# Kernel tuning notes

Measured on AMD Instinct MI355X. Metric: run time of the kernel, lower is better.

The kernel has to match this reference:

```python
import jax, jax.numpy as jnp
import numpy as np

B, T, C = 8, 2048, 1024
EPS = 1e-6
NEG_INF = -2.0**32 + 1.0


def setup_inputs() -> dict:
    key = jax.random.key(0)
    ks = jax.random.split(key, 10)
    glorot = lambda k, shape: jax.random.normal(k, shape, jnp.float32) * np.sqrt(2.0 / (shape[0] + shape[1]))
    return {
        "queries": jax.random.normal(ks[0], (B, T, C), jnp.float32),
        "keys": jax.random.normal(ks[1], (B, T, C), jnp.float32),
        "key_masks": jnp.ones((B, T), jnp.float32),
        "query_masks": jnp.ones((B, T), jnp.float32),
        "u": glorot(ks[2], (C, C)),
        # d = GlorotNormal([C,C]) * eye(C) -> only the diagonal matters
        "d_diag": jnp.diag(glorot(ks[3], (C, C))),
        "W1": glorot(ks[4], (C, C)),
        "b1": jnp.zeros((C,), jnp.float32),
        "W2": glorot(ks[5], (C, C)),
        "b2": jnp.zeros((C,), jnp.float32),
        "ln1_gamma": jnp.ones((C,), jnp.float32),
        "ln1_beta": jnp.zeros((C,), jnp.float32),
    }


def reference(queries, keys, key_masks, query_masks, u, d_diag, W1, b1, W2, b2, ln1_gamma, ln1_beta):
    c = queries.shape[-1]
    # bilinear score: relu(Q u) diag(d) relu(K u)^T
    f1 = jax.nn.relu(jnp.einsum('btc,cd->btd', queries, u))   # [B,T,C]
    f2 = jax.nn.relu(jnp.einsum('bsc,cd->bsd', keys, u))      # [B,T,C]
    S = jnp.einsum('btd,bsd->bts', f1 * d_diag, f2)           # [B,Tq,Tk]
    scale = max(1.0, float(c) ** 0.5)
    S = S / scale
    # key mask: broadcast [B,Tk] over query axis
    S = jnp.where(key_masks[:, None, :] == 0, jnp.asarray(NEG_INF, S.dtype), S)
    attn = jax.nn.softmax(S, axis=-1)
    attn = attn * query_masks[:, :, None]
    # dropout_rate=0 -> identity; values = keys
    out = jnp.matmul(attn, keys) + queries
    # LayerNorm(eps=1e-6)
    mu = jnp.mean(out, axis=-1, keepdims=True)
    var = jnp.mean(jnp.square(out - mu), axis=-1, keepdims=True)
    out = (out - mu) * jax.lax.rsqrt(var + EPS) * ln1_gamma + ln1_beta
    # FFN: dense1 (relu) -> dense2
    h = jax.nn.relu(jnp.einsum('btc,cd->btd', out, W1) + b1)
    out2 = jnp.einsum('btc,cd->btd', h, W2) + b2
    # original returns hiddens = [queries, outputs]
    return (queries, out2)
```

## Files before the change

### kernel.cpp

```cpp
#include <hip/hip_runtime.h>
#include <stdint.h>

typedef unsigned short ushort_t;
typedef __bf16 bf16x8 __attribute__((ext_vector_type(8)));
typedef float f32x4 __attribute__((ext_vector_type(4)));
typedef unsigned short us8 __attribute__((ext_vector_type(8)));
typedef unsigned short us4 __attribute__((ext_vector_type(4)));

#define BB 8
#define TT 2048
#define CC 1024
#define NEG_INF_F (-4294967295.0f)

__device__ __forceinline__ float bf2f(ushort_t u) {
    union { unsigned int i; float f; } v; v.i = ((unsigned int)u) << 16; return v.f;
}
__device__ __forceinline__ ushort_t f2bf(float f) {
    union { float f; unsigned int i; } v; v.f = f;
    unsigned int r = (v.i + 0x7fffu + ((v.i >> 16) & 1u)) >> 16;
    return (ushort_t)r;
}

__device__ __forceinline__ void gl_lds16(const ushort_t* g, ushort_t* l)
{
    __builtin_amdgcn_global_load_lds(
        (__attribute__((address_space(1))) void*)(void*)(g),
        (__attribute__((address_space(3))) void*)(l),
        16, 0, 0);
}

#define TM 128
#define TN 128
#define BK 64

__global__ __launch_bounds__(256) void gemm_bt(
    const ushort_t* __restrict__ Am, long sAe, int lda,
    const ushort_t* __restrict__ Bm, long sBe, int ldb,
    void* __restrict__ Cm, long sCbBytes, int ldc, int outF32,
    int K, float alpha, int epi,
    const float* __restrict__ aux, long sAuxb, int ldaux)
{
    __shared__ ushort_t aT[TM * BK];
    __shared__ ushort_t bT[TN * BK];
    const int z = blockIdx.z;
    const ushort_t* A = Am + (long)z * sAe;
    const ushort_t* B = Bm + (long)z * sBe;
    char* Cb = (char*)Cm + (long)z * sCbBytes;
    const int m0 = blockIdx.y * TM, n0 = blockIdx.x * TN;
    const int tid = threadIdx.x;
    const int w = tid >> 6, lane = tid & 63;
    const int wm = w >> 1, wn = w & 1;
    const int l15 = lane & 15, q = lane >> 4;

    f32x4 acc[4][4] = {};

    const int srow = 32 * w + (lane >> 3);
    const int skc  = ((lane & 7) ^ (lane >> 3)) * 8;
    const ushort_t* Ag = A + (long)(m0 + srow) * lda + skc;
    const ushort_t* Bg = B + (long)(n0 + srow) * ldb + skc;
    ushort_t* aL = aT + (32 * w) * BK;
    ushort_t* bL = bT + (32 * w) * BK;

    const int sw8 = l15 & 7;

    for (int k0 = 0; k0 < K; k0 += BK) {
        __syncthreads();
        #pragma unroll
        for (int t = 0; t < 4; t++) {
            gl_lds16(Ag + (long)(8 * t) * lda + k0, aL + (8 * t) * BK);
            gl_lds16(Bg + (long)(8 * t) * ldb + k0, bL + (8 * t) * BK);
        }
        __syncthreads();
        #pragma unroll
        for (int ks = 0; ks < 2; ks++) {
            const int so = ((ks * 4 + q) ^ sw8) * 8;
            bf16x8 af[4], bfr[4];
            #pragma unroll
            for (int i = 0; i < 4; i++)
                af[i] = *(bf16x8*)(aT + (wm * 64 + i * 16 + l15) * BK + so);
            #pragma unroll
            for (int j = 0; j < 4; j++)
                bfr[j] = *(bf16x8*)(bT + (wn * 64 + j * 16 + l15) * BK + so);
            #pragma unroll
            for (int i = 0; i < 4; i++)
                #pragma unroll
                for (int j = 0; j < 4; j++)
                    acc[i][j] = __builtin_amdgcn_mfma_f32_16x16x32_bf16(af[i], bfr[j], acc[i][j], 0, 0, 0);
        }
    }

    #pragma unroll
    for (int i = 0; i < 4; i++) {
        #pragma unroll
        for (int r = 0; r < 4; r++) {
            const int row = m0 + wm * 64 + i * 16 + q * 4 + r;
            #pragma unroll
            for (int j = 0; j < 4; j++) {
                const int col = n0 + wn * 64 + j * 16 + l15;
                float v = acc[i][j][r] * alpha;
                if (epi == 1) v = fmaxf(v, 0.0f);
                else if (epi == 2) v = fmaxf(v, 0.0f) * aux[col];
                else if (epi == 3) v = v + aux[col];
                else if (epi == 4) v = fmaxf(v + aux[col], 0.0f);
                else if (epi == 5) v = v + aux[(long)z * sAuxb + (long)row * ldaux + col];
                if (outF32) ((float*)Cb)[(long)row * ldc + col] = v;
                else        ((ushort_t*)Cb)[(long)row * ldc + col] = f2bf(v);
            }
        }
    }
}

__global__ __launch_bounds__(256) void cast_f32_bf16_k(
    const float* __restrict__ in, ushort_t* __restrict__ out, int n8)
{
    const int i = blockIdx.x * 256 + threadIdx.x;
    if (i < n8) {
        float4 a = *(const float4*)(in + (long)i * 8);
        float4 b = *(const float4*)(in + (long)i * 8 + 4);
        us8 o;
        o[0] = f2bf(a.x); o[1] = f2bf(a.y); o[2] = f2bf(a.z); o[3] = f2bf(a.w);
        o[4] = f2bf(b.x); o[5] = f2bf(b.y); o[6] = f2bf(b.z); o[7] = f2bf(b.w);
        *(us8*)(out + (long)i * 8) = o;
    }
}

__global__ __launch_bounds__(256) void transpose_f32_bf16(
    const float* __restrict__ in, ushort_t* __restrict__ out,
    int R, int Cn, long sIn, long sOut)
{
    __shared__ ushort_t tile[32][33];
    in += (long)blockIdx.z * sIn;
    out += (long)blockIdx.z * sOut;
    const int c0 = blockIdx.x * 32, r0 = blockIdx.y * 32;
    const int tx = threadIdx.x & 31, ty = threadIdx.x >> 5;
    #pragma unroll
    for (int i = 0; i < 4; i++)
        tile[ty + i * 8][tx] = f2bf(in[(long)(r0 + ty + i * 8) * Cn + c0 + tx]);
    __syncthreads();
    #pragma unroll
    for (int i = 0; i < 4; i++)
        out[(long)(c0 + ty + i * 8) * R + r0 + tx] = tile[tx][ty + i * 8];
}

__global__ __launch_bounds__(256) void softmax_k(
    ushort_t* __restrict__ S, const float* __restrict__ km, const float* __restrict__ qm)
{
    const long row = blockIdx.x;
    const int b = (int)(row >> 11);
    ushort_t* Sr = S + row * TT;
    const int tid = threadIdx.x;
    us8 sv = *(us8*)(Sr + tid * 8);
    const float* kmr = km + (long)b * TT + tid * 8;
    float4 k0 = *(const float4*)kmr, k1 = *(const float4*)(kmr + 4);
    float kmv[8] = {k0.x, k0.y, k0.z, k0.w, k1.x, k1.y, k1.z, k1.w};
    float v[8];
    #pragma unroll
    for (int j = 0; j < 8; j++)
        v[j] = (kmv[j] == 0.0f) ? NEG_INF_F : bf2f(sv[j]);
    float mx = v[0];
    #pragma unroll
    for (int j = 1; j < 8; j++) mx = fmaxf(mx, v[j]);
    #pragma unroll
    for (int off = 32; off > 0; off >>= 1) mx = fmaxf(mx, __shfl_xor(mx, off));
    __shared__ float red[8];
    if ((tid & 63) == 0) red[tid >> 6] = mx;
    __syncthreads();
    mx = fmaxf(fmaxf(red[0], red[1]), fmaxf(red[2], red[3]));
    float e[8], s = 0.0f;
    #pragma unroll
    for (int j = 0; j < 8; j++) { e[j] = __expf(v[j] - mx); s += e[j]; }
    #pragma unroll
    for (int off = 32; off > 0; off >>= 1) s += __shfl_xor(s, off);
    if ((tid & 63) == 0) red[4 + (tid >> 6)] = s;
    __syncthreads();
    s = red[4] + red[5] + red[6] + red[7];
    const float scale = qm[row] / s;
    us8 o;
    #pragma unroll
    for (int j = 0; j < 8; j++) o[j] = f2bf(e[j] * scale);
    *(us8*)(Sr + tid * 8) = o;
}

__global__ __launch_bounds__(256) void ln_k(
    const ushort_t* __restrict__ olin, ushort_t* __restrict__ outp,
    const float* __restrict__ gamma, const float* __restrict__ beta)
{
    const long row = blockIdx.x;
    const ushort_t* xr = olin + row * CC;
    const int tid = threadIdx.x;
    us4 xq = *(const us4*)(xr + tid * 4);
    float xs[4] = {bf2f(xq[0]), bf2f(xq[1]), bf2f(xq[2]), bf2f(xq[3])};
    float s = xs[0] + xs[1] + xs[2] + xs[3];
    float ss = xs[0]*xs[0] + xs[1]*xs[1] + xs[2]*xs[2] + xs[3]*xs[3];
    #pragma unroll
    for (int off = 32; off > 0; off >>= 1) { s += __shfl_xor(s, off); ss += __shfl_xor(ss, off); }
    __shared__ float red[8];
    if ((tid & 63) == 0) { red[tid >> 6] = s; red[4 + (tid >> 6)] = ss; }
    __syncthreads();
    s = red[0] + red[1] + red[2] + red[3];
    ss = red[4] + red[5] + red[6] + red[7];
    const float mu = s * (1.0f / CC);
    const float var = ss * (1.0f / CC) - mu * mu;
    const float rstd = rsqrtf(var + 1e-6f);
    float4 gv = *(const float4*)(gamma + tid * 4);
    float4 bv = *(const float4*)(beta + tid * 4);
    float gs[4] = {gv.x, gv.y, gv.z, gv.w}, bs[4] = {bv.x, bv.y, bv.z, bv.w};
    us4 o;
    #pragma unroll
    for (int j = 0; j < 4; j++)
        o[j] = f2bf((xs[j] - mu) * rstd * gs[j] + bs[j]);
    *(us4*)(outp + row * CC + tid * 4) = o;
}

extern "C" void kernel_launch(void* const* d_in, const int* in_sizes, int n_in,
                              void* d_out, int out_size, void* d_ws, size_t ws_size,
                              hipStream_t stream)
{
    const float* queries     = (const float*)d_in[0];
    const float* keys        = (const float*)d_in[1];
    const float* key_masks   = (const float*)d_in[2];
    const float* query_masks = (const float*)d_in[3];
    const float* u           = (const float*)d_in[4];
    const float* dd          = (const float*)d_in[5];
    const float* W1          = (const float*)d_in[6];
    const float* b1          = (const float*)d_in[7];
    const float* W2          = (const float*)d_in[8];
    const float* b2          = (const float*)d_in[9];
    const float* g1          = (const float*)d_in[10];
    const float* be1         = (const float*)d_in[11];

    char* ws = (char*)d_ws;
    const long MiB = 1 << 20;
    ushort_t* f1    = (ushort_t*)(ws + 0 * MiB);
    ushort_t* f2    = (ushort_t*)(ws + 32 * MiB);
    ushort_t* uT    = (ushort_t*)(ws + 64 * MiB);
    ushort_t* Qbf   = (ushort_t*)(ws + 66 * MiB);
    ushort_t* Kbf   = (ushort_t*)(ws + 66 * MiB);
    ushort_t* S     = (ushort_t*)(ws + 64 * MiB);
    ushort_t* keysT = (ushort_t*)(ws + 0 * MiB);
    ushort_t* olin  = (ushort_t*)(ws + 32 * MiB);
    ushort_t* W1T   = (ushort_t*)(ws + 0 * MiB);
    ushort_t* W2T   = (ushort_t*)(ws + 2 * MiB);
    ushort_t* lnb   = (ushort_t*)(ws + 64 * MiB);
    ushort_t* hb    = (ushort_t*)(ws + 96 * MiB);
    (void)in_sizes; (void)n_in; (void)out_size; (void)ws_size;

    const int N8 = BB * TT * CC / 8;

    hipMemcpyAsync(d_out, d_in[0], (size_t)BB * TT * CC * sizeof(float),
                   hipMemcpyDeviceToDevice, stream);

    transpose_f32_bf16<<<dim3(CC / 32, CC / 32, 1), 256, 0, stream>>>(u, uT, CC, CC, 0, 0);

    cast_f32_bf16_k<<<N8 / 256, 256, 0, stream>>>(queries, Qbf, N8);
    gemm_bt<<<dim3(CC / TN, (BB * TT) / TM, 1), 256, 0, stream>>>(
        Qbf, 0, CC, uT, 0, CC, f1, 0, CC, 0, CC, 1.0f, 2, dd, 0, 0);
    cast_f32_bf16_k<<<N8 / 256, 256, 0, stream>>>(keys, Kbf, N8);
    gemm_bt<<<dim3(CC / TN, (BB * TT) / TM, 1), 256, 0, stream>>>(
        Kbf, 0, CC, uT, 0, CC, f2, 0, CC, 0, CC, 1.0f, 1, nullptr, 0, 0);
    gemm_bt<<<dim3(TT / TN, TT / TM, BB), 256, 0, stream>>>(
        f1, (long)TT * CC, CC, f2, (long)TT * CC, CC,
        S, (long)TT * TT * 2, TT, 0, CC, 1.0f / 32.0f, 0, nullptr, 0, 0);
    softmax_k<<<BB * TT, 256, 0, stream>>>(S, key_masks, query_masks);
    transpose_f32_bf16<<<dim3(CC / 32, TT / 32, BB), 256, 0, stream>>>(
        keys, keysT, TT, CC, (long)TT * CC, (long)CC * TT);
    gemm_bt<<<dim3(CC / TN, TT / TM, BB), 256, 0, stream>>>(
        S, (long)TT * TT, TT, keysT, (long)CC * TT, TT,
        olin, (long)TT * CC * 2, CC, 0, TT, 1.0f, 5, queries, (long)TT * CC, CC);
    transpose_f32_bf16<<<dim3(CC / 32, CC / 32, 1), 256, 0, stream>>>(W1, W1T, CC, CC, 0, 0);
    transpose_f32_bf16<<<dim3(CC / 32, CC / 32, 1), 256, 0, stream>>>(W2, W2T, CC, CC, 0, 0);
    ln_k<<<BB * TT, 256, 0, stream>>>(olin, lnb, g1, be1);
    gemm_bt<<<dim3(CC / TN, (BB * TT) / TM, 1), 256, 0, stream>>>(
        lnb, 0, CC, W1T, 0, CC, hb, 0, CC, 0, CC, 1.0f, 4, b1, 0, 0);
    gemm_bt<<<dim3(CC / TN, (BB * TT) / TM, 1), 256, 0, stream>>>(
        hb, 0, CC, W2T, 0, CC, (float*)d_out + (long)BB * TT * CC, 0, CC, 1,
        CC, 1.0f, 3, b2, 0, 0);
}
```

Before: 845.5 us.

## Rewrite GEMM as 256x256 tile with 8 waves and double-buffered LDS prefetch

Replaces the 128x128, 4-wave GEMM with a 256x256 tile using 8 waves and an LDS split into half-K slices. Global-to-LDS loads for the next one or two K-steps are issued between MFMA groups, using explicit vmcnt/lgkmcnt waits, barriers and setprio. This targets the load/compute serialisation of the old single-buffer loop and raises per-block data reuse. In exchange it uses more LDS (128 KB per block) and more accumulator registers. The larger tiles also give fewer blocks for the smaller GEMMs, and the LDS layout drops the old XOR swizzle, which may cause bank conflicts.

```diff
diff --git a/kernel.cpp b/kernel.cpp
--- a/kernel.cpp
+++ b/kernel.cpp
@@ -29,75 +29,123 @@
         16, 0, 0);
 }
 
-#define TM 128
-#define TN 128
-#define BK 64
-
-__global__ __launch_bounds__(256) void gemm_bt(
+#define BM 256
+#define BN 256
+#define BKT 64
+#define HKK 32
+
+__global__ __launch_bounds__(512, 2) void gemm_bt(
     const ushort_t* __restrict__ Am, long sAe, int lda,
     const ushort_t* __restrict__ Bm, long sBe, int ldb,
     void* __restrict__ Cm, long sCbBytes, int ldc, int outF32,
     int K, float alpha, int epi,
     const float* __restrict__ aux, long sAuxb, int ldaux)
 {
-    __shared__ ushort_t aT[TM * BK];
-    __shared__ ushort_t bT[TN * BK];
+    __shared__ ushort_t lds[8][256 * HKK];
     const int z = blockIdx.z;
     const ushort_t* A = Am + (long)z * sAe;
     const ushort_t* B = Bm + (long)z * sBe;
     char* Cb = (char*)Cm + (long)z * sCbBytes;
-    const int m0 = blockIdx.y * TM, n0 = blockIdx.x * TN;
+    const int m0 = blockIdx.y * BM, n0 = blockIdx.x * BN;
     const int tid = threadIdx.x;
     const int w = tid >> 6, lane = tid & 63;
-    const int wm = w >> 1, wn = w & 1;
+    const int wm = w >> 2, wn = w & 3;
     const int l15 = lane & 15, q = lane >> 4;
 
-    f32x4 acc[4][4] = {};
-
-    const int srow = 32 * w + (lane >> 3);
-    const int skc  = ((lane & 7) ^ (lane >> 3)) * 8;
-    const ushort_t* Ag = A + (long)(m0 + srow) * lda + skc;
-    const ushort_t* Bg = B + (long)(n0 + srow) * ldb + skc;
-    ushort_t* aL = aT + (32 * w) * BK;
-    ushort_t* bL = bT + (32 * w) * BK;
-
-    const int sw8 = l15 & 7;
-
-    for (int k0 = 0; k0 < K; k0 += BK) {
-        __syncthreads();
-        #pragma unroll
-        for (int t = 0; t < 4; t++) {
-            gl_lds16(Ag + (long)(8 * t) * lda + k0, aL + (8 * t) * BK);
-            gl_lds16(Bg + (long)(8 * t) * ldb + k0, bL + (8 * t) * BK);
-        }
-        __syncthreads();
-        #pragma unroll
-        for (int ks = 0; ks < 2; ks++) {
-            const int so = ((ks * 4 + q) ^ sw8) * 8;
-            bf16x8 af[4], bfr[4];
+    f32x4 acc[8][4] = {};
+
+    const int srow = w * 16 + (lane >> 2);
+    const int skoff = (lane & 3) * 8;
+    const ushort_t* Ag = A + (long)(m0 + srow) * lda + skoff;
+    const ushort_t* Bg = B + (long)(n0 + srow) * ldb + skoff;
+
+#define STAGE_A(c, h, tk) do { \
+    const ushort_t* _g = Ag + (long)(tk) * BKT + (h) * HKK; \
+    ushort_t* _l = &lds[(c) * 4 + (h)][w * 512]; \
+    gl_lds16(_g, _l); \
+    gl_lds16(_g + (long)128 * lda, _l + 4096); } while (0)
+#define STAGE_B(c, h, tk) do { \
+    const ushort_t* _g = Bg + (long)(tk) * BKT + (h) * HKK; \
+    ushort_t* _l = &lds[(c) * 4 + 2 + (h)][w * 512]; \
+    gl_lds16(_g, _l); \
+    gl_lds16(_g + (long)128 * ldb, _l + 4096); } while (0)
+#define RD_A(c, h, mf) (*(const bf16x8*)&lds[(c) * 4 + (h)][(wm * 128 + (mf) * 16 + l15) * HKK + q * 8])
+#define RD_B(c, h, nf) (*(const bf16x8*)&lds[(c) * 4 + 2 + (h)][(wn * 64 + (nf) * 16 + l15) * HKK + q * 8])
+#define FENCE() asm volatile("" ::: "memory")
+#define BARRIER() do { FENCE(); __builtin_amdgcn_s_barrier(); FENCE(); } while (0)
+#define WAIT_LGKM0() do { asm volatile("s_waitcnt lgkmcnt(0)" ::: "memory"); \
+                          __builtin_amdgcn_sched_barrier(0); } while (0)
+#define MFMA16(mbase) do { \
+    __builtin_amdgcn_s_setprio(1); \
+    _Pragma("unroll") \
+    for (int _i = 0; _i < 4; _i++) \
+        _Pragma("unroll") \
+        for (int _j = 0; _j < 4; _j++) \
+            acc[(mbase) + _i][_j] = __builtin_amdgcn_mfma_f32_16x16x32_bf16( \
+                af[_i], bfr[_j], acc[(mbase) + _i][_j], 0, 0, 0); \
+    __builtin_amdgcn_s_setprio(0); } while (0)
+
+    const int NT = K >> 6;
+
+    STAGE_A(0, 0, 0); STAGE_B(0, 0, 0);
+    STAGE_A(0, 1, 0); STAGE_B(0, 1, 0);
+    STAGE_A(1, 0, 1); STAGE_B(1, 0, 1);
+    asm volatile("s_waitcnt vmcnt(4)" ::: "memory");
+    BARRIER();
+
+    bf16x8 af[4], bfr[4];
+    for (int tk = 0; tk < NT; ++tk) {
+        const int c = tk & 1;
+        const int pf1 = (tk + 1 < NT), pf2 = (tk + 2 < NT);
+
+        #pragma unroll
+        for (int i = 0; i < 4; i++) af[i] = RD_A(c, 0, i);
+        #pragma unroll
+        for (int j = 0; j < 4; j++) bfr[j] = RD_B(c, 0, j);
+        if (pf1) STAGE_A(c ^ 1, 1, tk + 1);
+        BARRIER();
+        WAIT_LGKM0();
+        MFMA16(0);
+        BARRIER();
+
+        #pragma unroll
+        for (int i = 0; i < 4; i++) af[i] = RD_A(c, 0, 4 + i);
+        if (pf1) STAGE_B(c ^ 1, 1, tk + 1);
+        BARRIER();
+        WAIT_LGKM0();
+        MFMA16(4);
+        BARRIER();
+
+        #pragma unroll
+        for (int i = 0; i < 4; i++) af[i] = RD_A(c, 1, i);
+        #pragma unroll
+        for (int j = 0; j < 4; j++) bfr[j] = RD_B(c, 1, j);
+        if (pf2) STAGE_A(c, 0, tk + 2);
+        BARRIER();
+        WAIT_LGKM0();
+        MFMA16(0);
+        BARRIER();
+
+        #pragma unroll
+        for (int i = 0; i < 4; i++) af[i] = RD_A(c, 1, 4 + i);
+        if (pf2) STAGE_B(c, 0, tk + 2);
+        if (tk < NT - 2) asm volatile("s_waitcnt vmcnt(4)" ::: "memory");
+        else             asm volatile("s_waitcnt vmcnt(0)" ::: "memory");
+        BARRIER();
+        WAIT_LGKM0();
+        MFMA16(4);
+        BARRIER();
+    }
+
+    #pragma unroll
+    for (int mf = 0; mf < 8; mf++) {
+        #pragma unroll
+        for (int r = 0; r < 4; r++) {
+            const int row = m0 + wm * 128 + mf * 16 + q * 4 + r;
             #pragma unroll
-            for (int i = 0; i < 4; i++)
-                af[i] = *(bf16x8*)(aT + (wm * 64 + i * 16 + l15) * BK + so);
-            #pragma unroll
-            for (int j = 0; j < 4; j++)
-                bfr[j] = *(bf16x8*)(bT + (wn * 64 + j * 16 + l15) * BK + so);
-            #pragma unroll
-            for (int i = 0; i < 4; i++)
-                #pragma unroll
-                for (int j = 0; j < 4; j++)
-                    acc[i][j] = __builtin_amdgcn_mfma_f32_16x16x32_bf16(af[i], bfr[j], acc[i][j], 0, 0, 0);
-        }
-    }
-
-    #pragma unroll
-    for (int i = 0; i < 4; i++) {
-        #pragma unroll
-        for (int r = 0; r < 4; r++) {
-            const int row = m0 + wm * 64 + i * 16 + q * 4 + r;
-            #pragma unroll
-            for (int j = 0; j < 4; j++) {
-                const int col = n0 + wn * 64 + j * 16 + l15;
-                float v = acc[i][j][r] * alpha;
+            for (int nf = 0; nf < 4; nf++) {
+                const int col = n0 + wn * 64 + nf * 16 + l15;
+                float v = acc[mf][nf][r] * alpha;
                 if (epi == 1) v = fmaxf(v, 0.0f);
                 else if (epi == 2) v = fmaxf(v, 0.0f) * aux[col];
                 else if (epi == 3) v = v + aux[col];
@@ -108,6 +156,14 @@
             }
         }
     }
+#undef STAGE_A
+#undef STAGE_B
+#undef RD_A
+#undef RD_B
+#undef FENCE
+#undef BARRIER
+#undef WAIT_LGKM0
+#undef MFMA16
 }
 
 __global__ __launch_bounds__(256) void cast_f32_bf16_k(
@@ -253,26 +309,26 @@
     transpose_f32_bf16<<<dim3(CC / 32, CC / 32, 1), 256, 0, stream>>>(u, uT, CC, CC, 0, 0);
 
     cast_f32_bf16_k<<<N8 / 256, 256, 0, stream>>>(queries, Qbf, N8);
-    gemm_bt<<<dim3(CC / TN, (BB * TT) / TM, 1), 256, 0, stream>>>(
+    gemm_bt<<<dim3(CC / BN, (BB * TT) / BM, 1), 512, 0, stream>>>(
         Qbf, 0, CC, uT, 0, CC, f1, 0, CC, 0, CC, 1.0f, 2, dd, 0, 0);
     cast_f32_bf16_k<<<N8 / 256, 256, 0, stream>>>(keys, Kbf, N8);
-    gemm_bt<<<dim3(CC / TN, (BB * TT) / TM, 1), 256, 0, stream>>>(
+    gemm_bt<<<dim3(CC / BN, (BB * TT) / BM, 1), 512, 0, stream>>>(
         Kbf, 0, CC, uT, 0, CC, f2, 0, CC, 0, CC, 1.0f, 1, nullptr, 0, 0);
-    gemm_bt<<<dim3(TT / TN, TT / TM, BB), 256, 0, stream>>>(
+    gemm_bt<<<dim3(TT / BN, TT / BM, BB), 512, 0, stream>>>(
         f1, (long)TT * CC, CC, f2, (long)TT * CC, CC,
         S, (long)TT * TT * 2, TT, 0, CC, 1.0f / 32.0f, 0, nullptr, 0, 0);
     softmax_k<<<BB * TT, 256, 0, stream>>>(S, key_masks, query_masks);
     transpose_f32_bf16<<<dim3(CC / 32, TT / 32, BB), 256, 0, stream>>>(
         keys, keysT, TT, CC, (long)TT * CC, (long)CC * TT);
-    gemm_bt<<<dim3(CC / TN, TT / TM, BB), 256, 0, stream>>>(
+    gemm_bt<<<dim3(CC / BN, TT / BM, BB), 512, 0, stream>>>(
         S, (long)TT * TT, TT, keysT, (long)CC * TT, TT,
         olin, (long)TT * CC * 2, CC, 0, TT, 1.0f, 5, queries, (long)TT * CC, CC);
     transpose_f32_bf16<<<dim3(CC / 32, CC / 32, 1), 256, 0, stream>>>(W1, W1T, CC, CC, 0, 0);
     transpose_f32_bf16<<<dim3(CC / 32, CC / 32, 1), 256, 0, stream>>>(W2, W2T, CC, CC, 0, 0);
     ln_k<<<BB * TT, 256, 0, stream>>>(olin, lnb, g1, be1);
-    gemm_bt<<<dim3(CC / TN, (BB * TT) / TM, 1), 256, 0, stream>>>(
+    gemm_bt<<<dim3(CC / BN, (BB * TT) / BM, 1), 512, 0, stream>>>(
         lnb, 0, CC, W1T, 0, CC, hb, 0, CC, 0, CC, 1.0f, 4, b1, 0, 0);
-    gemm_bt<<<dim3(CC / TN, (BB * TT) / TM, 1), 256, 0, stream>>>(
+    gemm_bt<<<dim3(CC / BN, (BB * TT) / BM, 1), 512, 0, stream>>>(
         hb, 0, CC, W2T, 0, CC, (float*)d_out + (long)BB * TT * CC, 0, CC, 1,
         CC, 1.0f, 3, b2, 0, 0);
 }
```

Result: faster. 745.0 us (-11.9%).
